# Kernel optimization log

Hardware: AMD Instinct MI355X
Metric: run time of the kernel (lower is better)

Reference implementation:

```python
import jax, jax.numpy as jnp
import numpy as np

NEG = -9e15   # mask value used by reference pyGAT implementation
ALPHA = 0.2   # LeakyReLU negative slope
B, N, F_IN, H, F_HID = 131072, 8, 30, 3, 8


def setup_inputs() -> dict:
    key = jax.random.key(0)
    ks = jax.random.split(key, 14)
    x = jax.random.normal(ks[0], (B, N, F_IN), jnp.float32)
    adj = (jax.random.uniform(ks[1], (B, N, N)) > 0.5).astype(jnp.float32)
    adj = jnp.maximum(adj, jnp.eye(N, dtype=jnp.float32))  # self loops

    def init(k, shp, fan):
        return jax.random.normal(k, shp, jnp.float32) * np.float32(1.0 / np.sqrt(fan))

    return {
        "x": x,
        "adj": adj,
        "W_heads": init(ks[2], (H, F_IN, F_HID), F_IN),       # per-head W
        "a_heads": init(ks[3], (H, 2 * F_HID), 2 * F_HID),    # per-head attention vec
        "W_out": init(ks[4], (H * F_HID, 1), H * F_HID),      # out_att W (nclass=1)
        "a_out": init(ks[5], (2,), 2),                          # out_att attention vec
        "mu_W": init(ks[6], (8, 8), 8), "mu_b": jnp.zeros((8,), jnp.float32),
        "sg_W": init(ks[7], (8, 8), 8), "sg_b": jnp.zeros((8,), jnp.float32),
        "v_W": init(ks[8], (1, 8), 8), "v_b": jnp.zeros((1,), jnp.float32),
    }


def _gat(x, adj, W_heads, a_heads, W_out, a_out):
    # --- multi-head layer (concat=True) ---
    Wh = jnp.einsum('bnf,hfo->bhno', x, W_heads)            # [B,H,N,F_HID]
    a1, a2 = a_heads[:, :F_HID], a_heads[:, F_HID:]
    f1 = jnp.einsum('bhno,ho->bhn', Wh, a1)
    f2 = jnp.einsum('bhno,ho->bhn', Wh, a2)
    e = jax.nn.leaky_relu(f1[:, :, :, None] + f2[:, :, None, :], ALPHA)  # [B,H,N,N]
    e = jnp.where(adj[:, None, :, :] > 0, e, NEG)
    att = jax.nn.softmax(e, axis=-1)
    h = jax.nn.elu(jnp.einsum('bhnm,bhmo->bhno', att, Wh))  # [B,H,N,F_HID]
    h = h.transpose(0, 2, 1, 3).reshape(x.shape[0], N, H * F_HID)  # concat heads

    # --- output attention layer (concat=False, nclass=1) ---
    Wh2 = h @ W_out                                          # [B,N,1]
    g1 = Wh2[..., 0] * a_out[0]
    g2 = Wh2[..., 0] * a_out[1]
    e2 = jax.nn.leaky_relu(g1[:, :, None] + g2[:, None, :], ALPHA)  # [B,N,N]
    e2 = jnp.where(adj > 0, e2, NEG)
    att2 = jax.nn.softmax(e2, axis=-1)
    out = jnp.einsum('bnm,bmo->bno', att2, Wh2)              # [B,N,1]
    return jax.nn.elu(out)[..., 0]                            # squeeze(-1) -> [B,8]


def reference(x, adj, W_heads, a_heads, W_out, a_out,
              mu_W, mu_b, sg_W, sg_b, v_W, v_b):
    g = _gat(x, adj, W_heads, a_heads, W_out, a_out)          # [B,8]
    mu = jax.nn.sigmoid(g @ mu_W.T + mu_b)                    # [B,8]
    sigma = jax.nn.softplus(g @ sg_W.T + sg_b) + 0.001        # [B,8]
    value = g @ v_W.T + v_b                                   # [B,1]
    return (mu, sigma, value)
```

## Files before the change

kernel.cpp:

```cpp
#include <hip/hip_runtime.h>
#include <math.h>

#define TPB 256

constexpr int Bn    = 131072;
constexpr float LOG2E = 1.4426950408889634f;

typedef float v2f __attribute__((ext_vector_type(2)));

__global__ __launch_bounds__(TPB)
void gat_ppo_kernel(const float* __restrict__ xg,
                    const float* __restrict__ adjg,
                    const float* __restrict__ Wg,
                    const float* __restrict__ ahg,
                    const float* __restrict__ wog,
                    const float* __restrict__ aog,
                    const float* __restrict__ muWg,
                    const float* __restrict__ mubg,
                    const float* __restrict__ sgWg,
                    const float* __restrict__ sgbg,
                    const float* __restrict__ vWg,
                    const float* __restrict__ vbg,
                    float* __restrict__ outg)
{
    __shared__ float xs[TPB * 30];

    const int lb = threadIdx.x;
    const int w  = lb >> 6;
    const int wl = lb & 63;
    const int g  = wl >> 3;
    const int n  = lb & 7;
    const int t  = blockIdx.x * TPB + lb;

    float* slice = xs + w * (64 * 30);

    {
        const float2* src = (const float2*)(xg)
                          + (size_t)blockIdx.x * (TPB * 15) + w * (64 * 15);
        float2* dst = (float2*)slice;
        #pragma unroll
        for (int k = 0; k < 15; ++k)
            dst[wl + k * 64] = src[wl + k * 64];
    }

    unsigned amask;
    {
        const float4* a4 = (const float4*)(adjg) + (size_t)t * 2;
        float4 a0 = a4[0], a1 = a4[1];
        amask =  (unsigned)(a0.x > 0.0f)
              | ((unsigned)(a0.y > 0.0f) << 1)
              | ((unsigned)(a0.z > 0.0f) << 2)
              | ((unsigned)(a0.w > 0.0f) << 3)
              | ((unsigned)(a1.x > 0.0f) << 4)
              | ((unsigned)(a1.y > 0.0f) << 5)
              | ((unsigned)(a1.z > 0.0f) << 6)
              | ((unsigned)(a1.w > 0.0f) << 7);
    }

    float x[30];
    {
        const float2* xr = (const float2*)slice + wl * 15;
        #pragma unroll
        for (int k = 0; k < 15; ++k) {
            float2 v = xr[k];
            x[2 * k] = v.x; x[2 * k + 1] = v.y;
        }
    }

    float4* wt4 = (float4*)slice;
    const v2f* Wp = (const v2f*)Wg;
    float wh2 = 0.0f;

    #pragma unroll
    for (int h = 0; h < 3; ++h) {
        v2f acc[4];
        #pragma unroll
        for (int o2 = 0; o2 < 4; ++o2) acc[o2] = (v2f){0.0f, 0.0f};
        #pragma unroll
        for (int f = 0; f < 30; ++f) {
            v2f xf = (v2f){x[f], x[f]};
            #pragma unroll
            for (int o2 = 0; o2 < 4; ++o2)
                acc[o2] = __builtin_elementwise_fma(xf, Wp[h * 120 + f * 4 + o2], acc[o2]);
        }

        float s1 = 0.0f, s2 = 0.0f;
        #pragma unroll
        for (int o2 = 0; o2 < 4; ++o2) {
            s1 = fmaf(acc[o2].x, ahg[h * 16 + 2 * o2],     s1);
            s1 = fmaf(acc[o2].y, ahg[h * 16 + 2 * o2 + 1], s1);
            s2 = fmaf(acc[o2].x, ahg[h * 16 + 8 + 2 * o2],     s2);
            s2 = fmaf(acc[o2].y, ahg[h * 16 + 8 + 2 * o2 + 1], s2);
        }
        float f1h = s1 * LOG2E;
        float f2h = s2 * LOG2E;

        wt4[g * 25 + n * 3]     = (float4){acc[0].x, acc[0].y, acc[1].x, acc[1].y};
        wt4[g * 25 + n * 3 + 1] = (float4){acc[2].x, acc[2].y, acc[3].x, acc[3].y};

        float p[8];
        float s = 0.0f;
        #pragma unroll
        for (int m = 0; m < 8; ++m) {
            float ev = f1h + __shfl(f2h, m, 8);
            ev = (ev > 0.0f) ? ev : 0.2f * ev;
            float pe = ((amask >> m) & 1u) ? __builtin_amdgcn_exp2f(ev) : 0.0f;
            p[m] = pe; s += pe;
        }
        float rs = 1.0f / s;

        v2f hacc[4];
        #pragma unroll
        for (int o2 = 0; o2 < 4; ++o2) hacc[o2] = (v2f){0.0f, 0.0f};
        #pragma unroll
        for (int m = 0; m < 8; ++m) {
            float4 lo = wt4[g * 25 + m * 3];
            float4 hi = wt4[g * 25 + m * 3 + 1];
            float attm = p[m] * rs;
            v2f av = (v2f){attm, attm};
            hacc[0] = __builtin_elementwise_fma(av, (v2f){lo.x, lo.y}, hacc[0]);
            hacc[1] = __builtin_elementwise_fma(av, (v2f){lo.z, lo.w}, hacc[1]);
            hacc[2] = __builtin_elementwise_fma(av, (v2f){hi.x, hi.y}, hacc[2]);
            hacc[3] = __builtin_elementwise_fma(av, (v2f){hi.z, hi.w}, hacc[3]);
        }
        #pragma unroll
        for (int o2 = 0; o2 < 4; ++o2) {
            #pragma unroll
            for (int j = 0; j < 2; ++j) {
                float hv = hacc[o2][j];
                hv = (hv > 0.0f) ? hv : (__expf(hv) - 1.0f);
                wh2 = fmaf(hv, wog[h * 8 + 2 * o2 + j], wh2);
            }
        }
    }

    const float a0c = aog[0] * LOG2E, a1c = aog[1] * LOG2E;
    float wh2a[8];
    #pragma unroll
    for (int m = 0; m < 8; ++m) wh2a[m] = __shfl(wh2, m, 8);

    float g1 = a0c * wh2;
    float p2[8];
    float s2s = 0.0f;
    #pragma unroll
    for (int m = 0; m < 8; ++m) {
        float ev = fmaf(a1c, wh2a[m], g1);
        ev = (ev > 0.0f) ? ev : 0.2f * ev;
        float pe = ((amask >> m) & 1u) ? __builtin_amdgcn_exp2f(ev) : 0.0f;
        p2[m] = pe; s2s += pe;
    }
    float rs2 = 1.0f / s2s;
    float og = 0.0f;
    #pragma unroll
    for (int m = 0; m < 8; ++m) og = fmaf(p2[m] * rs2, wh2a[m], og);
    float g2v = (og > 0.0f) ? og : (__expf(og) - 1.0f);

    float gall[8];
    #pragma unroll
    for (int m = 0; m < 8; ++m) gall[m] = __shfl(g2v, m, 8);

    float mu = mubg[n];
    float sg = sgbg[n];
    float vv = vbg[0];
    #pragma unroll
    for (int k = 0; k < 8; ++k) {
        mu = fmaf(gall[k], muWg[n * 8 + k], mu);
        sg = fmaf(gall[k], sgWg[n * 8 + k], sg);
        vv = fmaf(gall[k], vWg[k],          vv);
    }
    mu = 1.0f / (1.0f + __expf(-mu));
    sg = fmaxf(sg, 0.0f) + log1pf(__expf(-fabsf(sg))) + 0.001f;

    outg[t]          = mu;
    outg[Bn * 8 + t] = sg;
    if (n == 0) outg[Bn * 16 + (t >> 3)] = vv;
}

extern "C" void kernel_launch(void* const* d_in, const int* in_sizes, int n_in,
                              void* d_out, int out_size, void* d_ws, size_t ws_size,
                              hipStream_t stream) {
    const float* xg   = (const float*)d_in[0];
    const float* adjg = (const float*)d_in[1];
    const float* Wg   = (const float*)d_in[2];
    const float* ahg  = (const float*)d_in[3];
    const float* wog  = (const float*)d_in[4];
    const float* aog  = (const float*)d_in[5];
    const float* muW  = (const float*)d_in[6];
    const float* mub  = (const float*)d_in[7];
    const float* sgW  = (const float*)d_in[8];
    const float* sgb  = (const float*)d_in[9];
    const float* vW   = (const float*)d_in[10];
    const float* vb   = (const float*)d_in[11];
    float* outg = (float*)d_out;

    dim3 grid(Bn * 8 / TPB);
    gat_ppo_kernel<<<grid, TPB, 0, stream>>>(xg, adjg, Wg, ahg, wog, aog,
                                             muW, mub, sgW, sgb, vW, vb, outg);
}
```

Baseline: 50.56 us.

## Load x directly from global, shrink LDS tile, defer softmax normalization

Drops the coalesced staging of x through shared memory. Each thread now reads its own 30-float row straight from global, and the LDS allocation shrinks to a per-wave Wh tile, which should raise occupancy. It also defers the softmax division until after the attention-weighted sums, fuses the second-layer softmax and aggregation into one loop, uses fmax for LeakyReLU, and packs the final linear heads into v2f FMAs. The direct per-thread row loads are strided (120 bytes apart across lanes), so coalescing gets worse, which matters in a memory-bound kernel.

```diff
diff --git a/kernel.cpp b/kernel.cpp
--- a/kernel.cpp
+++ b/kernel.cpp
@@ -23,25 +23,15 @@
                     const float* __restrict__ vbg,
                     float* __restrict__ outg)
 {
-    __shared__ float xs[TPB * 30];
+    __shared__ float4 tile[4 * 200];
 
     const int lb = threadIdx.x;
     const int w  = lb >> 6;
-    const int wl = lb & 63;
-    const int g  = wl >> 3;
+    const int g  = (lb & 63) >> 3;
     const int n  = lb & 7;
     const int t  = blockIdx.x * TPB + lb;
 
-    float* slice = xs + w * (64 * 30);
-
-    {
-        const float2* src = (const float2*)(xg)
-                          + (size_t)blockIdx.x * (TPB * 15) + w * (64 * 15);
-        float2* dst = (float2*)slice;
-        #pragma unroll
-        for (int k = 0; k < 15; ++k)
-            dst[wl + k * 64] = src[wl + k * 64];
-    }
+    float4* wt4 = tile + w * 200;
 
     unsigned amask;
     {
@@ -59,7 +49,7 @@
 
     float x[30];
     {
-        const float2* xr = (const float2*)slice + wl * 15;
+        const float2* xr = (const float2*)(xg + (size_t)t * 30);
         #pragma unroll
         for (int k = 0; k < 15; ++k) {
             float2 v = xr[k];
@@ -67,7 +57,6 @@
         }
     }
 
-    float4* wt4 = (float4*)slice;
     const v2f* Wp = (const v2f*)Wg;
     float wh2 = 0.0f;
 
@@ -103,11 +92,10 @@
         #pragma unroll
         for (int m = 0; m < 8; ++m) {
             float ev = f1h + __shfl(f2h, m, 8);
-            ev = (ev > 0.0f) ? ev : 0.2f * ev;
+            ev = fmaxf(ev, 0.2f * ev);
             float pe = ((amask >> m) & 1u) ? __builtin_amdgcn_exp2f(ev) : 0.0f;
             p[m] = pe; s += pe;
         }
-        float rs = 1.0f / s;
 
         v2f hacc[4];
         #pragma unroll
@@ -116,18 +104,18 @@
         for (int m = 0; m < 8; ++m) {
             float4 lo = wt4[g * 25 + m * 3];
             float4 hi = wt4[g * 25 + m * 3 + 1];
-            float attm = p[m] * rs;
-            v2f av = (v2f){attm, attm};
+            v2f av = (v2f){p[m], p[m]};
             hacc[0] = __builtin_elementwise_fma(av, (v2f){lo.x, lo.y}, hacc[0]);
             hacc[1] = __builtin_elementwise_fma(av, (v2f){lo.z, lo.w}, hacc[1]);
             hacc[2] = __builtin_elementwise_fma(av, (v2f){hi.x, hi.y}, hacc[2]);
             hacc[3] = __builtin_elementwise_fma(av, (v2f){hi.z, hi.w}, hacc[3]);
         }
+        float rs = 1.0f / s;
         #pragma unroll
         for (int o2 = 0; o2 < 4; ++o2) {
             #pragma unroll
             for (int j = 0; j < 2; ++j) {
-                float hv = hacc[o2][j];
+                float hv = hacc[o2][j] * rs;
                 hv = (hv > 0.0f) ? hv : (__expf(hv) - 1.0f);
                 wh2 = fmaf(hv, wog[h * 8 + 2 * o2 + j], wh2);
             }
@@ -140,34 +128,38 @@
     for (int m = 0; m < 8; ++m) wh2a[m] = __shfl(wh2, m, 8);
 
     float g1 = a0c * wh2;
-    float p2[8];
     float s2s = 0.0f;
+    float og = 0.0f;
     #pragma unroll
     for (int m = 0; m < 8; ++m) {
         float ev = fmaf(a1c, wh2a[m], g1);
-        ev = (ev > 0.0f) ? ev : 0.2f * ev;
+        ev = fmaxf(ev, 0.2f * ev);
         float pe = ((amask >> m) & 1u) ? __builtin_amdgcn_exp2f(ev) : 0.0f;
-        p2[m] = pe; s2s += pe;
+        s2s += pe;
+        og = fmaf(pe, wh2a[m], og);
     }
-    float rs2 = 1.0f / s2s;
-    float og = 0.0f;
-    #pragma unroll
-    for (int m = 0; m < 8; ++m) og = fmaf(p2[m] * rs2, wh2a[m], og);
+    og /= s2s;
     float g2v = (og > 0.0f) ? og : (__expf(og) - 1.0f);
 
-    float gall[8];
+    v2f gp[4];
     #pragma unroll
-    for (int m = 0; m < 8; ++m) gall[m] = __shfl(g2v, m, 8);
+    for (int m = 0; m < 4; ++m)
+        gp[m] = (v2f){__shfl(g2v, 2 * m, 8), __shfl(g2v, 2 * m + 1, 8)};
 
-    float mu = mubg[n];
-    float sg = sgbg[n];
-    float vv = vbg[0];
+    const v2f* muWp = (const v2f*)muWg;
+    const v2f* sgWp = (const v2f*)sgWg;
+    const v2f* vWp  = (const v2f*)vWg;
+    v2f ma = (v2f){0.0f, 0.0f}, sa = (v2f){0.0f, 0.0f}, va = (v2f){0.0f, 0.0f};
     #pragma unroll
-    for (int k = 0; k < 8; ++k) {
-        mu = fmaf(gall[k], muWg[n * 8 + k], mu);
-        sg = fmaf(gall[k], sgWg[n * 8 + k], sg);
-        vv = fmaf(gall[k], vWg[k],          vv);
+    for (int k = 0; k < 4; ++k) {
+        ma = __builtin_elementwise_fma(gp[k], muWp[n * 4 + k], ma);
+        sa = __builtin_elementwise_fma(gp[k], sgWp[n * 4 + k], sa);
+        va = __builtin_elementwise_fma(gp[k], vWp[k],          va);
     }
+    float mu = ma.x + ma.y + mubg[n];
+    float sg = sa.x + sa.y + sgbg[n];
+    float vv = va.x + va.y + vbg[0];
+
     mu = 1.0f / (1.0f + __expf(-mu));
     sg = fmaxf(sg, 0.0f) + log1pf(__expf(-fabsf(sg))) + 0.001f;
 
```

New measurement: 50.37 us. No clear change (-0.4%).
